# Kernel optimization log

Measured on AMD Instinct MI355X. Metric: run time of the kernel, lower is better.

## Reference

```python
import jax, jax.numpy as jnp
import numpy as np

THR = 0.5      # span-selection threshold
K_SUBJ = 16    # max subject/object spans kept per sentence (padded)
K_OBJ = 8      # max object spans kept per (subject, relation)

# Greedy threshold-based span pairing: for each start position i with
# start_prob>THR, take the first unused j>=i with end_prob>THR (NMS-like).
# Returns fixed-size padded spans [K,2] (int32) and a validity mask [K].
def greedy_spans(sp, ep, K):
    S = sp.shape[0]
    idxs = jnp.arange(S, dtype=jnp.int32)
    def step(carry, i):
        used, count, spans, valid = carry
        gate = sp[i] > THR
        cand = (ep > THR) & (~used) & (idxs >= i)
        has = jnp.any(cand)
        j = jnp.argmax(cand).astype(jnp.int32)  # first True
        found = gate & has
        slot = jnp.minimum(count, K - 1)
        write = found & (count < K)
        pair = jnp.where(write, jnp.stack([i, j]).astype(jnp.int32), spans[slot])
        spans = spans.at[slot].set(pair)
        valid = valid.at[slot].set(valid[slot] | write)
        used = used.at[j].set(used[j] | found)
        count = count + found.astype(jnp.int32)
        return (used, count, spans, valid), None
    init = (jnp.zeros(S, bool), jnp.int32(0),
            jnp.zeros((K, 2), jnp.int32), jnp.zeros(K, bool))
    (_, _, spans, valid), _ = jax.lax.scan(step, init, idxs)
    return spans, valid


def _model(token_embs, hg, rel_embs, b_rel_transe, head_w, head_b,
           Wmats, Wbias, rproj_w, rproj_b, V_w, V_b):
    # head_w/head_b order: 0 start_subj, 1 end_subj, 2 b_start_obj, 3 b_end_obj,
    #                      4 start_obj, 5 end_obj, 6 b_start_subj, 7 b_end_subj
    # Wmats/Wbias order:   0 W_s, 1 W_r, 2 W_g, 3 W_x, 4 W_r_b, 5 W_g_b, 6 W_x_b, 7 W_x2
    sig = jax.nn.sigmoid
    head = lambda x, i: sig(x @ head_w[i] + head_b[i])        # H->1 sigmoid head
    lin = lambda x, i: x @ Wmats[i].T + Wbias[i]              # H->H linear

    # ---- first-level span scores + greedy extraction (forward & backward) ----
    sub_sp, sub_ep = head(token_embs, 0), head(token_embs, 1)   # [B,S]
    bob_sp, bob_ep = head(token_embs, 2), head(token_embs, 3)
    g = jax.vmap(lambda a, b: greedy_spans(a, b, K_SUBJ))
    subj_spans, subj_valid = g(sub_sp, sub_ep)                  # [B,K,2],[B,K]
    b_subj_spans, b_subj_valid = g(bob_sp, bob_ep)

    def gather(tok_b, spans, valid):  # mean of start/end token embeddings
        e = (tok_b[spans[:, 0]] + tok_b[spans[:, 1]]) * 0.5
        return e * valid[:, None].astype(tok_b.dtype)
    s_k = jax.vmap(gather)(token_embs, subj_spans, subj_valid)      # [B,K,H]
    b_s_k = jax.vmap(gather)(token_embs, b_subj_spans, b_subj_valid)
    s_k_w = lin(s_k, 0) * subj_valid[..., None]                     # W_s + mask
    b_s_k_w = lin(b_s_k, 0) * b_subj_valid[..., None]

    # ---- relation-aware attention context C = sum_s A[b,s,r] * x[b,s] ----
    b_rel = b_rel_transe @ rproj_w.T + rproj_b                      # r_proj
    def attend(rels, ir, ig, ix):
        e = jnp.tanh(lin(token_embs, ix)[:, :, None, :]             # [B,S,1,H]
                     + lin(hg, ig)[:, None, None, :]                # [B,1,1,H]
                     + lin(rels, ir)[None, None, :, :])             # [1,1,R,H]
        v = e @ V_w + V_b[0]                                        # [B,S,R]
        A = jax.nn.softmax(v, axis=1)                               # over seq
        return jnp.einsum('bsr,bsh->brh', A, token_embs)            # [B,R,H]
    C = attend(rel_embs, 1, 2, 3)
    b_C = attend(b_rel, 4, 5, 6)

    # Heads are linear, so distribute w over the sum instead of
    # materializing the [B,S,K,R,H] tensor.
    tok_mix = token_embs + lin(token_embs, 7)
    def pair_probs(Cmat, skw, i):
        t_tok = tok_mix @ head_w[i]                                 # [B,S]
        t_sub = skw @ head_w[i]                                     # [B,K]
        t_rel = Cmat @ head_w[i]                                    # [B,R]
        return sig(t_tok[:, :, None, None] + t_sub[:, None, :, None]
                   + t_rel[:, None, None, :] + head_b[i])           # [B,S,K,R]
    obj_sp, obj_ep = pair_probs(C, s_k_w, 4), pair_probs(C, s_k_w, 5)
    bsub_sp, bsub_ep = pair_probs(b_C, b_s_k_w, 6), pair_probs(b_C, b_s_k_w, 7)

    # ---- greedy object-span extraction per (batch, subject, relation) ----
    def triples(sp4, ep4, subj_ok):
        B_, S_, K_, R_ = sp4.shape
        fsp = sp4.transpose(0, 2, 3, 1).reshape(-1, S_)
        fep = ep4.transpose(0, 2, 3, 1).reshape(-1, S_)
        spans, valid = jax.vmap(lambda a, b: greedy_spans(a, b, K_OBJ))(fsp, fep)
        spans = spans.reshape(B_, K_, R_, K_OBJ, 2)
        valid = valid.reshape(B_, K_, R_, K_OBJ) & subj_ok[:, :, None, None]
        return spans, valid
    f_spans, f_valid = triples(obj_sp, obj_ep, subj_valid)
    bw_spans, bw_valid = triples(bsub_sp, bsub_ep, b_subj_valid)

    probs = jnp.stack([obj_sp, obj_ep, bsub_sp, bsub_ep])           # [4,B,S,K,R]
    return (probs, subj_spans, subj_valid, b_subj_spans, b_subj_valid,
            f_spans, f_valid, bw_spans, bw_valid)


def setup_inputs() -> dict:
    key = jax.random.key(0)
    ks = jax.random.split(key, 12)
    B, S, H, R, T = 8, 256, 768, 40, 80
    sc = H ** -0.5
    return {
        'token_embs': jax.random.normal(ks[0], (B, S, H), jnp.float32),
        'hg': jax.random.normal(ks[1], (B, H), jnp.float32),
        'rel_embs': jax.random.normal(ks[2], (R, H), jnp.float32),
        'b_rel_transe': jax.random.normal(ks[3], (R, T), jnp.float32),
        'head_w': jax.random.normal(ks[4], (8, H), jnp.float32) * sc,
        'head_b': jax.random.normal(ks[5], (8,), jnp.float32) * 0.1,
        'Wmats': jax.random.normal(ks[6], (8, H, H), jnp.float32) * sc,
        'Wbias': jax.random.normal(ks[7], (8, H), jnp.float32) * 0.02,
        'rproj_w': jax.random.normal(ks[8], (H, T), jnp.float32) * (T ** -0.5),
        'rproj_b': jax.random.normal(ks[9], (H,), jnp.float32) * 0.02,
        'V_w': jax.random.normal(ks[10], (H,), jnp.float32) * sc,
        'V_b': jax.random.normal(ks[11], (1,), jnp.float32) * 0.1,
    }


def reference(token_embs, hg, rel_embs, b_rel_transe, head_w, head_b,
              Wmats, Wbias, rproj_w, rproj_b, V_w, V_b):
    return _model(token_embs, hg, rel_embs, b_rel_transe, head_w, head_b,
                  Wmats, Wbias, rproj_w, rproj_b, V_w, V_b)
```

## Files before the change

### kernel.cpp

```cpp
#include <hip/hip_runtime.h>
#include <hip/hip_bf16.h>
#include <stdint.h>

#define Bc 8
#define Sc 256
#define Hc 768
#define Rc 40
#define Tc 80
#define KSc 16
#define KOc 8

#define OUT_SSP 5242880
#define OUT_SVA 5243136
#define OUT_BSP 5243264
#define OUT_BVA 5243520
#define OUT_FSP 5243648
#define OUT_FVA 5325568
#define OUT_WSP 5366528
#define OUT_WVA 5448448

#define CM_PS (16 * Rc * Hc)
#define BSH (Bc * Sc * Hc)

__device__ inline double wave_reduce_d(double v) {
#pragma unroll
  for (int o = 32; o; o >>= 1) v += __shfl_down(v, o, 64);
  return v;
}
__device__ inline float wave_reduce_f(float v) {
#pragma unroll
  for (int o = 32; o; o >>= 1) v += __shfl_down(v, o, 64);
  return v;
}

__global__ __launch_bounds__(256) void k_prep0(const float* __restrict__ brt,
                                               const float* __restrict__ rw,
                                               const float* __restrict__ rb,
                                               const float* __restrict__ Wmats,
                                               const float* __restrict__ head_w,
                                               float* __restrict__ brel,
                                               double* __restrict__ hv) {
  int bb = blockIdx.x;
  int tid = threadIdx.x;
  if (bb < 12) {
    int idx = bb * 256 + tid;
    int i = idx / Hc, j = idx % Hc;
    const float* h4 = head_w + (4 + i) * Hc;
    const float* W7 = Wmats + (size_t)7 * Hc * Hc;
    double acc = (double)h4[j];
    for (int hh = 0; hh < Hc; ++hh)
      acc += (double)W7[(size_t)hh * Hc + j] * (double)h4[hh];
    hv[idx] = acc;
  } else {
    int idx = (bb - 12) * 256 + tid;
    int r = idx / Hc, h = idx % Hc;
    float acc = rb[h];
    const float* a = brt + r * Tc;
    const float* w = rw + (size_t)h * Tc;
    for (int t = 0; t < Tc; ++t) acc = fmaf(a[t], w[t], acc);
    brel[idx] = acc;
  }
}

__global__ __launch_bounds__(256) void k_l03tt(const float* __restrict__ x,
                                               const float* __restrict__ head_w,
                                               const float* __restrict__ head_b,
                                               const double* __restrict__ hv,
                                               float* __restrict__ l03,
                                               double* __restrict__ tt) {
  int bs = blockIdx.x * 4 + (threadIdx.x >> 6);
  int lane = threadIdx.x & 63;
  if (bs >= Bc * Sc) return;
  const float* xr = x + (size_t)bs * Hc;
  double acc[8] = {0, 0, 0, 0, 0, 0, 0, 0};
  for (int h = lane; h < Hc; h += 64) {
    double xv = (double)xr[h];
    acc[0] += xv * (double)head_w[h];
    acc[1] += xv * (double)head_w[Hc + h];
    acc[2] += xv * (double)head_w[2 * Hc + h];
    acc[3] += xv * (double)head_w[3 * Hc + h];
    acc[4] += xv * hv[h];
    acc[5] += xv * hv[Hc + h];
    acc[6] += xv * hv[2 * Hc + h];
    acc[7] += xv * hv[3 * Hc + h];
  }
#pragma unroll
  for (int i = 0; i < 4; ++i) {
    double a = wave_reduce_d(acc[i]);
    if (lane == 0) l03[i * (Bc * Sc) + bs] = (float)(a + (double)head_b[i]);
  }
#pragma unroll
  for (int i = 0; i < 4; ++i) {
    double a = wave_reduce_d(acc[4 + i]);
    if (lane == 0) tt[i * (Bc * Sc) + bs] = a;
  }
}

__device__ inline int find_first(const uint64_t* epm, const uint64_t* used, int i) {
  int wi = i >> 6;
  uint64_t m = epm[wi] & ~used[wi] & (~0ull << (i & 63));
  if (m) return (wi << 6) + (__ffsll((unsigned long long)m) - 1);
  for (int w = wi + 1; w < 4; ++w) {
    uint64_t mm = epm[w] & ~used[w];
    if (mm) return (w << 6) + (__ffsll((unsigned long long)mm) - 1);
  }
  return -1;
}

__global__ __launch_bounds__(64) void k_greedy1(const float* __restrict__ l03,
                                                int* __restrict__ spans1, int* __restrict__ valid1,
                                                float* __restrict__ out) {
  int t = blockIdx.x;
  int dir = t >> 3, b = t & 7;
  int lane = threadIdx.x;
  const float* sp = l03 + (dir * 2) * (Bc * Sc) + b * Sc;
  const float* ep = sp + Bc * Sc;
  uint64_t spm[4], epm[4];
#pragma unroll
  for (int w = 0; w < 4; ++w) {
    spm[w] = __ballot(sp[w * 64 + lane] > 0.f);
    epm[w] = __ballot(ep[w * 64 + lane] > 0.f);
  }
  __shared__ int ssp0[KSc], ssp1[KSc], sva[KSc];
  if (lane < KSc) { ssp0[lane] = 0; ssp1[lane] = 0; sva[lane] = 0; }
  __syncthreads();
  if (lane == 0) {
    uint64_t used[4] = {0, 0, 0, 0};
    int cnt = 0;
#pragma unroll
    for (int w = 0; w < 4; ++w) {
      uint64_t g = spm[w];
      while (g) {
        int bit = __ffsll((unsigned long long)g) - 1;
        g &= g - 1;
        int i = w * 64 + bit;
        int j = find_first(epm, used, i);
        if (j < 0) continue;
        used[j >> 6] |= (1ull << (j & 63));
        if (cnt < KSc) { ssp0[cnt] = i; ssp1[cnt] = j; sva[cnt] = 1; }
        cnt++;
      }
    }
  }
  __syncthreads();
  int base = (dir * Bc + b) * KSc;
  float* osp = out + (dir ? OUT_BSP : OUT_SSP) + b * KSc * 2;
  float* ova = out + (dir ? OUT_BVA : OUT_SVA) + b * KSc;
  if (lane < KSc) {
    spans1[(base + lane) * 2] = ssp0[lane];
    spans1[(base + lane) * 2 + 1] = ssp1[lane];
    valid1[base + lane] = sva[lane];
    osp[lane * 2] = (float)ssp0[lane];
    osp[lane * 2 + 1] = (float)ssp1[lane];
    ova[lane] = (float)sva[lane];
  }
}

__global__ __launch_bounds__(256) void k_egather(const float* __restrict__ x,
                                                 const int* __restrict__ spans1,
                                                 float* __restrict__ eb) {
  int row = blockIdx.x;
  int b = (row / KSc) % Bc;
  int s0 = spans1[row * 2], s1 = spans1[row * 2 + 1];
  const float* x0 = x + ((size_t)b * Sc + s0) * Hc;
  const float* x1 = x + ((size_t)b * Sc + s1) * Hc;
  float* er = eb + (size_t)row * Hc;
  for (int h = threadIdx.x; h < Hc; h += 256) er[h] = 0.5f * (x0[h] + x1[h]);
}

__global__ __launch_bounds__(256) void k_small(const float* __restrict__ eb,
                                               const float* __restrict__ hg,
                                               const float* __restrict__ rel,
                                               const float* __restrict__ brel,
                                               const float* __restrict__ Wmats,
                                               const float* __restrict__ Wbias,
                                               const int* __restrict__ valid1,
                                               float* __restrict__ skw,
                                               float* __restrict__ tg,
                                               float* __restrict__ tr) {
  int bb = blockIdx.x;
  const float* Asrc; int M; int wsel; float* dst; int m0, n0; bool msk = false;
  if (bb < 96) {
    Asrc = eb; M = 256; wsel = 0; dst = skw; msk = true;
    m0 = (bb / 12) * 32; n0 = (bb % 12) * 64;
  } else {
    int q = bb - 96;
    if (q < 12)      { Asrc = hg;   M = 8;  wsel = 2; dst = tg;           m0 = 0; n0 = q * 64; }
    else if (q < 24) { Asrc = hg;   M = 8;  wsel = 5; dst = tg + 8 * Hc;  m0 = 0; n0 = (q - 12) * 64; }
    else if (q < 48) { int qq = q - 24; Asrc = rel;  M = 40; wsel = 1; dst = tr;           m0 = (qq / 12) * 32; n0 = (qq % 12) * 64; }
    else             { int qq = q - 48; Asrc = brel; M = 40; wsel = 4; dst = tr + 40 * Hc; m0 = (qq / 12) * 32; n0 = (qq % 12) * 64; }
  }
  const float* W = Wmats + (size_t)wsel * Hc * Hc;
  const float* bias = Wbias + wsel * Hc;
  __shared__ float Asl[32][36];
  __shared__ float Bsl[32][68];
  int tid = threadIdx.x;
  int arow = tid >> 3, acol = (tid & 7) << 2;
  int brow = tid >> 2, bcol = (tid & 3) << 2;
  int txi = tid & 15, tyi = tid >> 4;
  int ar = m0 + arow;
  const float* ap = Asrc + (size_t)(ar < M ? ar : 0) * Hc + acol;
  const float* bp = W + (size_t)(n0 + brow) * Hc + bcol;
  int nb = n0 + txi * 4;
  float4 bv = *(const float4*)&bias[nb];
  float acc[2][4];
#pragma unroll
  for (int i = 0; i < 2; ++i) { acc[i][0] = bv.x; acc[i][1] = bv.y; acc[i][2] = bv.z; acc[i][3] = bv.w; }
  for (int k0 = 0; k0 < Hc; k0 += 32) {
    float4 av = *(const float4*)(ap + k0);
    float4 b0 = *(const float4*)(bp + k0);
    float4 b1 = *(const float4*)(bp + k0 + 16);
    __syncthreads();
    Asl[acol + 0][arow] = av.x; Asl[acol + 1][arow] = av.y; Asl[acol + 2][arow] = av.z; Asl[acol + 3][arow] = av.w;
    Bsl[bcol + 0][brow] = b0.x; Bsl[bcol + 1][brow] = b0.y; Bsl[bcol + 2][brow] = b0.z; Bsl[bcol + 3][brow] = b0.w;
    Bsl[bcol + 16][brow] = b1.x; Bsl[bcol + 17][brow] = b1.y; Bsl[bcol + 18][brow] = b1.z; Bsl[bcol + 19][brow] = b1.w;
    __syncthreads();
#pragma unroll
    for (int kk = 0; kk < 32; ++kk) {
      float a0 = Asl[kk][tyi * 2], a1 = Asl[kk][tyi * 2 + 1];
      float4 b = *(const float4*)&Bsl[kk][txi * 4];
      acc[0][0] = fmaf(a0, b.x, acc[0][0]); acc[0][1] = fmaf(a0, b.y, acc[0][1]);
      acc[0][2] = fmaf(a0, b.z, acc[0][2]); acc[0][3] = fmaf(a0, b.w, acc[0][3]);
      acc[1][0] = fmaf(a1, b.x, acc[1][0]); acc[1][1] = fmaf(a1, b.y, acc[1][1]);
      acc[1][2] = fmaf(a1, b.z, acc[1][2]); acc[1][3] = fmaf(a1, b.w, acc[1][3]);
    }
  }
  int m_ = m0 + tyi * 2;
#pragma unroll
  for (int i = 0; i < 2; ++i) {
    int mrow = m_ + i;
    if (msk) {
      int v = valid1[mrow];
      float4 o;
      o.x = v ? acc[i][0] : 0.f; o.y = v ? acc[i][1] : 0.f;
      o.z = v ? acc[i][2] : 0.f; o.w = v ? acc[i][3] : 0.f;
      *(float4*)&dst[(size_t)mrow * Hc + nb] = o;
    } else if (mrow < M) {
      float4 o; o.x = acc[i][0]; o.y = acc[i][1]; o.z = acc[i][2]; o.w = acc[i][3];
      *(float4*)&dst[(size_t)mrow * Hc + nb] = o;
    }
  }
}

#define BM 64
#define BN 64
#define BKK 32
#define LDP 68
__global__ __launch_bounds__(256) void k_tx(const float* __restrict__ x,
                                            const float* __restrict__ Wmats,
                                            const float* __restrict__ Wbias,
                                            float* __restrict__ txo) {
  int dir = blockIdx.z;
  const float* W = Wmats + (size_t)(dir ? 6 : 3) * Hc * Hc;
  const float* bias = Wbias + (dir ? 6 : 3) * Hc;
  float* outp = txo + (size_t)dir * BSH;
  int m0 = blockIdx.y * BM;
  int n0 = blockIdx.x * BN;
  __shared__ float Asl[BKK][LDP];
  __shared__ float Bsl[BKK][LDP];
  int tid = threadIdx.x;
  int lr = tid >> 2;
  int lc = (tid & 3) << 2;
  int txi = tid & 15, tyi = tid >> 4;
  const float* xp = x + (size_t)(m0 + lr) * Hc + lc;
  const float* wp = W + (size_t)(n0 + lr) * Hc + lc;
  float4 a0 = *(const float4*)(xp);
  float4 a1 = *(const float4*)(xp + 16);
  float4 b0 = *(const float4*)(wp);
  float4 b1 = *(const float4*)(wp + 16);
  float acc[4][4] = {};
  for (int k0 = 0; k0 < Hc; k0 += BKK) {
    __syncthreads();
    Asl[lc + 0][lr] = a0.x; Asl[lc + 1][lr] = a0.y; Asl[lc + 2][lr] = a0.z; Asl[lc + 3][lr] = a0.w;
    Asl[lc + 16][lr] = a1.x; Asl[lc + 17][lr] = a1.y; Asl[lc + 18][lr] = a1.z; Asl[lc + 19][lr] = a1.w;
    Bsl[lc + 0][lr] = b0.x; Bsl[lc + 1][lr] = b0.y; Bsl[lc + 2][lr] = b0.z; Bsl[lc + 3][lr] = b0.w;
    Bsl[lc + 16][lr] = b1.x; Bsl[lc + 17][lr] = b1.y; Bsl[lc + 18][lr] = b1.z; Bsl[lc + 19][lr] = b1.w;
    __syncthreads();
    if (k0 + BKK < Hc) {
      a0 = *(const float4*)(xp + k0 + BKK);
      a1 = *(const float4*)(xp + k0 + BKK + 16);
      b0 = *(const float4*)(wp + k0 + BKK);
      b1 = *(const float4*)(wp + k0 + BKK + 16);
    }
#pragma unroll
    for (int kk = 0; kk < BKK; ++kk) {
      float4 a = *(const float4*)&Asl[kk][tyi * 4];
      float4 b = *(const float4*)&Bsl[kk][txi * 4];
      acc[0][0] = fmaf(a.x, b.x, acc[0][0]); acc[0][1] = fmaf(a.x, b.y, acc[0][1]);
      acc[0][2] = fmaf(a.x, b.z, acc[0][2]); acc[0][3] = fmaf(a.x, b.w, acc[0][3]);
      acc[1][0] = fmaf(a.y, b.x, acc[1][0]); acc[1][1] = fmaf(a.y, b.y, acc[1][1]);
      acc[1][2] = fmaf(a.y, b.z, acc[1][2]); acc[1][3] = fmaf(a.y, b.w, acc[1][3]);
      acc[2][0] = fmaf(a.z, b.x, acc[2][0]); acc[2][1] = fmaf(a.z, b.y, acc[2][1]);
      acc[2][2] = fmaf(a.z, b.z, acc[2][2]); acc[2][3] = fmaf(a.z, b.w, acc[2][3]);
      acc[3][0] = fmaf(a.w, b.x, acc[3][0]); acc[3][1] = fmaf(a.w, b.y, acc[3][1]);
      acc[3][2] = fmaf(a.w, b.z, acc[3][2]); acc[3][3] = fmaf(a.w, b.w, acc[3][3]);
    }
  }
  int nb = n0 + txi * 4;
  float4 bb = *(const float4*)&bias[nb];
#pragma unroll
  for (int i2 = 0; i2 < 4; ++i2) {
    float4 o;
    o.x = acc[i2][0] + bb.x; o.y = acc[i2][1] + bb.y;
    o.z = acc[i2][2] + bb.z; o.w = acc[i2][3] + bb.w;
    *(float4*)&outp[(size_t)(m0 + tyi * 4 + i2) * Hc + nb] = o;
  }
}

__global__ __launch_bounds__(256) void k_v(const float* __restrict__ txo,
                                           const float* __restrict__ tg,
                                           const float* __restrict__ tr,
                                           const float* __restrict__ Vw,
                                           const float* __restrict__ Vb,
                                           float* __restrict__ va) {
  const float Cl = 2.8853900817779268f;
  int id = blockIdx.x;
  int dir = id >> 10;
  int rem = id & 1023;
  int rhalf = rem & 1;
  int bs0 = (rem >> 1) * 4;
  int b = bs0 >> 8;
  int tid = threadIdx.x;
  int wv = tid >> 6, lane = tid & 63;
  const float* tgr = tg + (dir * Bc + b) * Hc;
  float xt[4][12], vw[12];
#pragma unroll
  for (int u = 0; u < 12; ++u) {
    int h = lane + 64 * u;
    vw[u] = Vw[h];
    float tgv = tgr[h];
#pragma unroll
    for (int si = 0; si < 4; ++si)
      xt[si][u] = (txo[((size_t)dir * (Bc * Sc) + bs0 + si) * Hc + h] + tgv) * Cl;
  }
  float vb0 = Vb[0];
  for (int q = 0; q < 5; ++q) {
    int r = rhalf * 20 + wv * 5 + q;
    const float* trr = tr + ((size_t)dir * Rc + r) * Hc + lane;
    float p0 = 0.f, p1 = 0.f, p2 = 0.f, p3 = 0.f;
#pragma unroll
    for (int u = 0; u < 12; ++u) {
      float t = trr[64 * u] * Cl;
      float e0 = __builtin_amdgcn_exp2f(xt[0][u] + t);
      float e1 = __builtin_amdgcn_exp2f(xt[1][u] + t);
      float e2 = __builtin_amdgcn_exp2f(xt[2][u] + t);
      float e3 = __builtin_amdgcn_exp2f(xt[3][u] + t);
      p0 = fmaf(fmaf(-2.f, __builtin_amdgcn_rcpf(e0 + 1.f), 1.f), vw[u], p0);
      p1 = fmaf(fmaf(-2.f, __builtin_amdgcn_rcpf(e1 + 1.f), 1.f), vw[u], p1);
      p2 = fmaf(fmaf(-2.f, __builtin_amdgcn_rcpf(e2 + 1.f), 1.f), vw[u], p2);
      p3 = fmaf(fmaf(-2.f, __builtin_amdgcn_rcpf(e3 + 1.f), 1.f), vw[u], p3);
    }
    p0 = wave_reduce_f(p0); p1 = wave_reduce_f(p1);
    p2 = wave_reduce_f(p2); p3 = wave_reduce_f(p3);
    if (lane == 0) {
      size_t base = ((size_t)dir * (Bc * Sc) + bs0) * Rc + r;
      va[base] = p0 + vb0;
      va[base + Rc] = p1 + vb0;
      va[base + 2 * Rc] = p2 + vb0;
      va[base + 3 * Rc] = p3 + vb0;
    }
  }
}

__global__ __launch_bounds__(256) void k_softmax(float* __restrict__ va) {
  int id = blockIdx.x;
  int dir = id / (Bc * Rc); int rem = id % (Bc * Rc);
  int b = rem / Rc; int r = rem % Rc;
  int s = threadIdx.x;
  float* base = va + (((size_t)dir * Bc + b) * Sc) * Rc + r;
  float v = base[(size_t)s * Rc];
  __shared__ float red[8];
  float m = v;
#pragma unroll
  for (int o = 32; o; o >>= 1) m = fmaxf(m, __shfl_xor(m, o, 64));
  if ((s & 63) == 0) red[s >> 6] = m;
  __syncthreads();
  if (s == 0) red[4] = fmaxf(fmaxf(red[0], red[1]), fmaxf(red[2], red[3]));
  __syncthreads();
  m = red[4];
  float e = expf(v - m);
  float t = e;
#pragma unroll
  for (int o = 32; o; o >>= 1) t += __shfl_xor(t, o, 64);
  __syncthreads();
  if ((s & 63) == 0) red[s >> 6] = t;
  __syncthreads();
  if (s == 0) red[4] = red[0] + red[1] + red[2] + red[3];
  __syncthreads();
  base[(size_t)s * Rc] = e / red[4];
}

__global__ __launch_bounds__(256, 1) void k_C(const float* __restrict__ va,
                                              const float* __restrict__ x,
                                              float* __restrict__ Cm4) {
  int id = blockIdx.x;
  int rr = id & 1;
  int p = (id >> 1) & 3;
  int g = id >> 3;
  int b = g & 7;
  __shared__ float As_[64 * Rc];
  int tid = threadIdx.x;
  const float* vab = va + ((size_t)g * Sc + p * 64) * Rc;
  for (int idx = tid; idx < 64 * Rc; idx += 256) As_[idx] = vab[idx];
  __syncthreads();
  const float* xb = x + ((size_t)b * Sc + p * 64) * Hc;
  float acc[3][20];
#pragma unroll
  for (int j = 0; j < 3; ++j)
#pragma unroll
    for (int r = 0; r < 20; ++r) acc[j][r] = 0.f;
  int rbase = rr * 20;
  for (int s = 0; s < 64; ++s) {
    float xv0 = xb[(size_t)s * Hc + tid];
    float xv1 = xb[(size_t)s * Hc + 256 + tid];
    float xv2 = xb[(size_t)s * Hc + 512 + tid];
#pragma unroll
    for (int q = 0; q < 5; ++q) {
      float4 a4 = *(const float4*)&As_[s * Rc + rbase + q * 4];
      acc[0][q * 4 + 0] = fmaf(a4.x, xv0, acc[0][q * 4 + 0]);
      acc[0][q * 4 + 1] = fmaf(a4.y, xv0, acc[0][q * 4 + 1]);
      acc[0][q * 4 + 2] = fmaf(a4.z, xv0, acc[0][q * 4 + 2]);
      acc[0][q * 4 + 3] = fmaf(a4.w, xv0, acc[0][q * 4 + 3]);
      acc[1][q * 4 + 0] = fmaf(a4.x, xv1, acc[1][q * 4 + 0]);
      acc[1][q * 4 + 1] = fmaf(a4.y, xv1, acc[1][q * 4 + 1]);
      acc[1][q * 4 + 2] = fmaf(a4.z, xv1, acc[1][q * 4 + 2]);
      acc[1][q * 4 + 3] = fmaf(a4.w, xv1, acc[1][q * 4 + 3]);
      acc[2][q * 4 + 0] = fmaf(a4.x, xv2, acc[2][q * 4 + 0]);
      acc[2][q * 4 + 1] = fmaf(a4.y, xv2, acc[2][q * 4 + 1]);
      acc[2][q * 4 + 2] = fmaf(a4.z, xv2, acc[2][q * 4 + 2]);
      acc[2][q * 4 + 3] = fmaf(a4.w, xv2, acc[2][q * 4 + 3]);
    }
  }
#pragma unroll
  for (int r = 0; r < 20; ++r) {
    size_t base = ((size_t)(p * 16 + g) * Rc + rbase + r) * Hc + tid;
    Cm4[base] = acc[0][r];
    Cm4[base + 256] = acc[1][r];
    Cm4[base + 512] = acc[2][r];
  }
}

__global__ __launch_bounds__(256) void k_tsc(const float* __restrict__ skw,
                                             const float* __restrict__ Cm4,
                                             const float* __restrict__ head_w,
                                             const float* __restrict__ Wbias,
                                             double* __restrict__ ts,
                                             double* __restrict__ trl,
                                             double* __restrict__ c4) {
  int wave = blockIdx.x * 4 + (threadIdx.x >> 6);
  int lane = threadIdx.x & 63;
  const float* src; const float* w; double* dst;
  bool partial4 = false;
  if (wave < 512) {
    int p = wave >> 7, rem = wave & 127;
    int b = rem >> 4, k = rem & 15, dir = p >> 1;
    src = skw + (((size_t)(dir * Bc + b)) * KSc + k) * Hc;
    w = head_w + (4 + p) * Hc;
    dst = ts + (p * Bc + b) * KSc + k;
  } else if (wave < 1792) {
    int q = wave - 512;
    int p = q / 320, rem = q % 320;
    int b = rem / Rc, r = rem % Rc, dir = p >> 1;
    src = Cm4 + ((size_t)(dir * Bc + b) * Rc + r) * Hc;
    w = head_w + (4 + p) * Hc;
    dst = trl + (p * Bc + b) * Rc + r;
    partial4 = true;
  } else if (wave < 1796) {
    int p = wave - 1792;
    src = Wbias + 7 * Hc;
    w = head_w + (4 + p) * Hc;
    dst = c4 + p;
  } else return;
  double acc = 0.0;
  if (partial4) {
    for (int h = lane; h < Hc; h += 64) {
      double cs = (double)src[h] + (double)src[h + CM_PS] +
                  (double)src[h + 2 * CM_PS] + (double)src[h + 3 * CM_PS];
      acc += cs * (double)w[h];
    }
  } else {
    for (int h = lane; h < Hc; h += 64) acc += (double)src[h] * (double)w[h];
  }
  acc = wave_reduce_d(acc);
  if (lane == 0) *dst = acc;
}

__global__ __launch_bounds__(256) void k_probs(const double* __restrict__ tt,
                                               const double* __restrict__ ts,
                                               const double* __restrict__ trl,
                                               const double* __restrict__ c4,
                                               const float* __restrict__ head_b,
                                               float* __restrict__ out) {
  const float L2E = 1.4426950408889634f;
  int id = blockIdx.x;
  int b = id >> 8, s = id & 255;
  (void)s;
  __shared__ double tsb[4][KSc];
  __shared__ double trb[4][Rc];
  __shared__ double basep[4];
  int tid = threadIdx.x;
  if (tid < 64) { int p = tid >> 4, k = tid & 15; tsb[p][k] = ts[(p * Bc + b) * KSc + k]; }
  if (tid < 160) { int p = tid / Rc, r = tid % Rc; trb[p][r] = trl[(p * Bc + b) * Rc + r]; }
  if (tid < 4) basep[tid] = tt[tid * (Bc * Sc) + id] + c4[tid] + (double)head_b[4 + tid];
  __syncthreads();
#pragma unroll
  for (int p = 0; p < 4; ++p) {
    double base = basep[p];
    float* op = out + ((size_t)(p * Bc) * Sc + id) * (KSc * Rc);
    for (int kr = tid; kr < KSc * Rc; kr += 256) {
      int k = kr / Rc, r = kr - k * Rc;
      float l = (float)(base + tsb[p][k] + trb[p][r]);
      float e = __builtin_amdgcn_exp2f(-L2E * l);
      op[kr] = __builtin_amdgcn_rcpf(1.f + e);
    }
  }
}

__global__ __launch_bounds__(64) void k_greedy2(const double* __restrict__ tt,
                                                const double* __restrict__ ts,
                                                const double* __restrict__ trl,
                                                const double* __restrict__ c4,
                                                const float* __restrict__ head_b,
                                                const int* __restrict__ valid1,
                                                float* __restrict__ out) {
  int gid = blockIdx.x * 64 + threadIdx.x;
  if (gid >= 2 * Bc * KSc * Rc) return;
  int dir = gid / (Bc * KSc * Rc);
  int rem = gid % (Bc * KSc * Rc);
  int b = rem / (KSc * Rc);
  int kr = rem % (KSc * Rc);
  int k = kr / Rc, r = kr % Rc;
  int p0 = dir * 2, p1 = p0 + 1;
  double off0 = ts[(p0 * Bc + b) * KSc + k] + trl[(p0 * Bc + b) * Rc + r] + c4[p0] + (double)head_b[4 + p0];
  double off1 = ts[(p1 * Bc + b) * KSc + k] + trl[(p1 * Bc + b) * Rc + r] + c4[p1] + (double)head_b[4 + p1];
  const double* t0 = tt + p0 * (Bc * Sc) + b * Sc;
  const double* t1 = tt + p1 * (Bc * Sc) + b * Sc;
  uint64_t spm[4], epm[4], used[4] = {0, 0, 0, 0};
#pragma unroll
  for (int w = 0; w < 4; ++w) {
    uint64_t ms = 0, me = 0;
    for (int bit = 0; bit < 64; ++bit) {
      int s = w * 64 + bit;
      if (t0[s] + off0 > 0.0) ms |= (1ull << bit);
      if (t1[s] + off1 > 0.0) me |= (1ull << bit);
    }
    spm[w] = ms; epm[w] = me;
  }
  float* osp = out + (dir ? OUT_WSP : OUT_FSP) + (size_t)rem * KOc * 2;
  float* ova = out + (dir ? OUT_WVA : OUT_FVA) + (size_t)rem * KOc;
  for (int o = 0; o < KOc; ++o) { osp[o * 2] = 0.f; osp[o * 2 + 1] = 0.f; ova[o] = 0.f; }
  float sval = valid1[(dir * Bc + b) * KSc + k] ? 1.f : 0.f;
  int cnt = 0;
  for (int w = 0; w < 4; ++w) {
    uint64_t g = spm[w];
    while (g) {
      int bit = __ffsll((unsigned long long)g) - 1;
      g &= g - 1;
      int i = w * 64 + bit;
      int j = find_first(epm, used, i);
      if (j < 0) continue;
      used[j >> 6] |= (1ull << (j & 63));
      if (cnt < KOc) { osp[cnt * 2] = (float)i; osp[cnt * 2 + 1] = (float)j; ova[cnt] = sval; }
      cnt++;
    }
  }
}

extern "C" void kernel_launch(void* const* d_in, const int* in_sizes, int n_in,
                              void* d_out, int out_size, void* d_ws, size_t ws_size,
                              hipStream_t stream) {
  (void)in_sizes; (void)n_in; (void)out_size; (void)ws_size;
  const float* x = (const float*)d_in[0];
  const float* hg = (const float*)d_in[1];
  const float* rel = (const float*)d_in[2];
  const float* brt = (const float*)d_in[3];
  const float* head_w = (const float*)d_in[4];
  const float* head_b = (const float*)d_in[5];
  const float* Wmats = (const float*)d_in[6];
  const float* Wbias = (const float*)d_in[7];
  const float* rproj_w = (const float*)d_in[8];
  const float* rproj_b = (const float*)d_in[9];
  const float* Vw = (const float*)d_in[10];
  const float* Vb = (const float*)d_in[11];
  float* out = (float*)d_out;
  char* ws = (char*)d_ws;

  double* hv  = (double*)(ws + 0);
  double* c4  = (double*)(ws + 24576);
  double* tt  = (double*)(ws + 24608);
  double* ts  = (double*)(ws + 90144);
  double* trl = (double*)(ws + 94240);
  float* l03  = (float*)(ws + 104480);
  float* brel = (float*)(ws + 137248);
  float* tg   = (float*)(ws + 260128);
  float* tr   = (float*)(ws + 309280);
  float* txb  = (float*)(ws + 555040);
  float* va   = (float*)(ws + 13137952);
  float* skw  = (float*)(ws + 15759392);
  int* spans1 = (int*)(ws + 16545824);
  int* valid1 = (int*)(ws + 16547872);
  float* eb   = txb;
  float* Cm4  = txb;

  k_prep0<<<132, 256, 0, stream>>>(brt, rproj_w, rproj_b, Wmats, head_w, brel, hv);
  k_l03tt<<<512, 256, 0, stream>>>(x, head_w, head_b, hv, l03, tt);
  k_greedy1<<<16, 64, 0, stream>>>(l03, spans1, valid1, out);
  k_egather<<<256, 256, 0, stream>>>(x, spans1, eb);
  k_small<<<168, 256, 0, stream>>>(eb, hg, rel, brel, Wmats, Wbias, valid1, skw, tg, tr);
  k_tx<<<dim3(12, 32, 2), 256, 0, stream>>>(x, Wmats, Wbias, txb);
  k_v<<<2048, 256, 0, stream>>>(txb, tg, tr, Vw, Vb, va);
  k_softmax<<<640, 256, 0, stream>>>(va);
  k_C<<<128, 256, 0, stream>>>(va, x, Cm4);
  k_tsc<<<449, 256, 0, stream>>>(skw, Cm4, head_w, Wbias, ts, trl, c4);
  k_probs<<<2048, 256, 0, stream>>>(tt, ts, trl, c4, head_b, out);
  k_greedy2<<<160, 64, 0, stream>>>(tt, ts, trl, c4, head_b, valid1, out);
}
```

Baseline: 310.3 us.

## Fuse span gather into GEMM load and merge probs with greedy2 kernel

Drops the separate span-embedding gather kernel by computing the average of the two endpoint token rows directly inside the k_small GEMM's A-tile load. The sigmoid-probability kernel and the second greedy extraction kernel are merged into one launch, with extra blocks handling the greedy work at 256 threads per block instead of 64. This removes two kernel launches and the intermediate buffer write and read. In exchange, the GEMM issues two global loads per A element, and the greedy threads are now packed into fewer, larger blocks.

```diff
diff --git a/kernel.cpp b/kernel.cpp
--- a/kernel.cpp
+++ b/kernel.cpp
@@ -156,19 +156,8 @@
   }
 }
 
-__global__ __launch_bounds__(256) void k_egather(const float* __restrict__ x,
-                                                 const int* __restrict__ spans1,
-                                                 float* __restrict__ eb) {
-  int row = blockIdx.x;
-  int b = (row / KSc) % Bc;
-  int s0 = spans1[row * 2], s1 = spans1[row * 2 + 1];
-  const float* x0 = x + ((size_t)b * Sc + s0) * Hc;
-  const float* x1 = x + ((size_t)b * Sc + s1) * Hc;
-  float* er = eb + (size_t)row * Hc;
-  for (int h = threadIdx.x; h < Hc; h += 256) er[h] = 0.5f * (x0[h] + x1[h]);
-}
-
-__global__ __launch_bounds__(256) void k_small(const float* __restrict__ eb,
+__global__ __launch_bounds__(256) void k_small(const float* __restrict__ x,
+                                               const int* __restrict__ spans1,
                                                const float* __restrict__ hg,
                                                const float* __restrict__ rel,
                                                const float* __restrict__ brel,
@@ -179,9 +168,9 @@
                                                float* __restrict__ tg,
                                                float* __restrict__ tr) {
   int bb = blockIdx.x;
-  const float* Asrc; int M; int wsel; float* dst; int m0, n0; bool msk = false;
+  const float* Asrc = nullptr; int M; int wsel; float* dst; int m0, n0; bool msk = false;
   if (bb < 96) {
-    Asrc = eb; M = 256; wsel = 0; dst = skw; msk = true;
+    M = 256; wsel = 0; dst = skw; msk = true;
     m0 = (bb / 12) * 32; n0 = (bb % 12) * 64;
   } else {
     int q = bb - 96;
@@ -199,7 +188,17 @@
   int brow = tid >> 2, bcol = (tid & 3) << 2;
   int txi = tid & 15, tyi = tid >> 4;
   int ar = m0 + arow;
-  const float* ap = Asrc + (size_t)(ar < M ? ar : 0) * Hc + acol;
+  const float* ap = nullptr;
+  const float* apA = nullptr;
+  const float* apB = nullptr;
+  if (msk) {
+    int s0 = spans1[ar * 2], s1 = spans1[ar * 2 + 1];
+    int b = (ar >> 4) & 7;
+    apA = x + ((size_t)b * Sc + s0) * Hc + acol;
+    apB = x + ((size_t)b * Sc + s1) * Hc + acol;
+  } else {
+    ap = Asrc + (size_t)(ar < M ? ar : 0) * Hc + acol;
+  }
   const float* bp = W + (size_t)(n0 + brow) * Hc + bcol;
   int nb = n0 + txi * 4;
   float4 bv = *(const float4*)&bias[nb];
@@ -207,7 +206,15 @@
 #pragma unroll
   for (int i = 0; i < 2; ++i) { acc[i][0] = bv.x; acc[i][1] = bv.y; acc[i][2] = bv.z; acc[i][3] = bv.w; }
   for (int k0 = 0; k0 < Hc; k0 += 32) {
-    float4 av = *(const float4*)(ap + k0);
+    float4 av;
+    if (msk) {
+      float4 u = *(const float4*)(apA + k0);
+      float4 v = *(const float4*)(apB + k0);
+      av.x = 0.5f * (u.x + v.x); av.y = 0.5f * (u.y + v.y);
+      av.z = 0.5f * (u.z + v.z); av.w = 0.5f * (u.w + v.w);
+    } else {
+      av = *(const float4*)(ap + k0);
+    }
     float4 b0 = *(const float4*)(bp + k0);
     float4 b1 = *(const float4*)(bp + k0 + 16);
     __syncthreads();
@@ -485,83 +492,78 @@
   if (lane == 0) *dst = acc;
 }
 
-__global__ __launch_bounds__(256) void k_probs(const double* __restrict__ tt,
-                                               const double* __restrict__ ts,
-                                               const double* __restrict__ trl,
-                                               const double* __restrict__ c4,
-                                               const float* __restrict__ head_b,
-                                               float* __restrict__ out) {
+__global__ __launch_bounds__(256) void k_post(const double* __restrict__ tt,
+                                              const double* __restrict__ ts,
+                                              const double* __restrict__ trl,
+                                              const double* __restrict__ c4,
+                                              const float* __restrict__ head_b,
+                                              const int* __restrict__ valid1,
+                                              float* __restrict__ out) {
   const float L2E = 1.4426950408889634f;
-  int id = blockIdx.x;
-  int b = id >> 8, s = id & 255;
-  (void)s;
-  __shared__ double tsb[4][KSc];
-  __shared__ double trb[4][Rc];
-  __shared__ double basep[4];
+  int bb = blockIdx.x;
   int tid = threadIdx.x;
-  if (tid < 64) { int p = tid >> 4, k = tid & 15; tsb[p][k] = ts[(p * Bc + b) * KSc + k]; }
-  if (tid < 160) { int p = tid / Rc, r = tid % Rc; trb[p][r] = trl[(p * Bc + b) * Rc + r]; }
-  if (tid < 4) basep[tid] = tt[tid * (Bc * Sc) + id] + c4[tid] + (double)head_b[4 + tid];
-  __syncthreads();
-#pragma unroll
-  for (int p = 0; p < 4; ++p) {
-    double base = basep[p];
-    float* op = out + ((size_t)(p * Bc) * Sc + id) * (KSc * Rc);
-    for (int kr = tid; kr < KSc * Rc; kr += 256) {
-      int k = kr / Rc, r = kr - k * Rc;
-      float l = (float)(base + tsb[p][k] + trb[p][r]);
-      float e = __builtin_amdgcn_exp2f(-L2E * l);
-      op[kr] = __builtin_amdgcn_rcpf(1.f + e);
-    }
-  }
-}
-
-__global__ __launch_bounds__(64) void k_greedy2(const double* __restrict__ tt,
-                                                const double* __restrict__ ts,
-                                                const double* __restrict__ trl,
-                                                const double* __restrict__ c4,
-                                                const float* __restrict__ head_b,
-                                                const int* __restrict__ valid1,
-                                                float* __restrict__ out) {
-  int gid = blockIdx.x * 64 + threadIdx.x;
-  if (gid >= 2 * Bc * KSc * Rc) return;
-  int dir = gid / (Bc * KSc * Rc);
-  int rem = gid % (Bc * KSc * Rc);
-  int b = rem / (KSc * Rc);
-  int kr = rem % (KSc * Rc);
-  int k = kr / Rc, r = kr % Rc;
-  int p0 = dir * 2, p1 = p0 + 1;
-  double off0 = ts[(p0 * Bc + b) * KSc + k] + trl[(p0 * Bc + b) * Rc + r] + c4[p0] + (double)head_b[4 + p0];
-  double off1 = ts[(p1 * Bc + b) * KSc + k] + trl[(p1 * Bc + b) * Rc + r] + c4[p1] + (double)head_b[4 + p1];
-  const double* t0 = tt + p0 * (Bc * Sc) + b * Sc;
-  const double* t1 = tt + p1 * (Bc * Sc) + b * Sc;
-  uint64_t spm[4], epm[4], used[4] = {0, 0, 0, 0};
-#pragma unroll
-  for (int w = 0; w < 4; ++w) {
-    uint64_t ms = 0, me = 0;
-    for (int bit = 0; bit < 64; ++bit) {
-      int s = w * 64 + bit;
-      if (t0[s] + off0 > 0.0) ms |= (1ull << bit);
-      if (t1[s] + off1 > 0.0) me |= (1ull << bit);
-    }
-    spm[w] = ms; epm[w] = me;
-  }
-  float* osp = out + (dir ? OUT_WSP : OUT_FSP) + (size_t)rem * KOc * 2;
-  float* ova = out + (dir ? OUT_WVA : OUT_FVA) + (size_t)rem * KOc;
-  for (int o = 0; o < KOc; ++o) { osp[o * 2] = 0.f; osp[o * 2 + 1] = 0.f; ova[o] = 0.f; }
-  float sval = valid1[(dir * Bc + b) * KSc + k] ? 1.f : 0.f;
-  int cnt = 0;
-  for (int w = 0; w < 4; ++w) {
-    uint64_t g = spm[w];
-    while (g) {
-      int bit = __ffsll((unsigned long long)g) - 1;
-      g &= g - 1;
-      int i = w * 64 + bit;
-      int j = find_first(epm, used, i);
-      if (j < 0) continue;
-      used[j >> 6] |= (1ull << (j & 63));
-      if (cnt < KOc) { osp[cnt * 2] = (float)i; osp[cnt * 2 + 1] = (float)j; ova[cnt] = sval; }
-      cnt++;
+  if (bb < 2048) {
+    int id = bb;
+    int b = id >> 8;
+    __shared__ double tsb[4][KSc];
+    __shared__ double trb[4][Rc];
+    __shared__ double basep[4];
+    if (tid < 64) { int p = tid >> 4, k = tid & 15; tsb[p][k] = ts[(p * Bc + b) * KSc + k]; }
+    if (tid < 160) { int p = tid / Rc, r = tid % Rc; trb[p][r] = trl[(p * Bc + b) * Rc + r]; }
+    if (tid < 4) basep[tid] = tt[tid * (Bc * Sc) + id] + c4[tid] + (double)head_b[4 + tid];
+    __syncthreads();
+#pragma unroll
+    for (int p = 0; p < 4; ++p) {
+      double base = basep[p];
+      float* op = out + ((size_t)(p * Bc) * Sc + id) * (KSc * Rc);
+      for (int kr = tid; kr < KSc * Rc; kr += 256) {
+        int k = kr / Rc, r = kr - k * Rc;
+        float l = (float)(base + tsb[p][k] + trb[p][r]);
+        float e = __builtin_amdgcn_exp2f(-L2E * l);
+        op[kr] = __builtin_amdgcn_rcpf(1.f + e);
+      }
+    }
+  } else {
+    int gid = (bb - 2048) * 256 + tid;
+    if (gid >= 2 * Bc * KSc * Rc) return;
+    int dir = gid / (Bc * KSc * Rc);
+    int rem = gid % (Bc * KSc * Rc);
+    int b = rem / (KSc * Rc);
+    int kr = rem % (KSc * Rc);
+    int k = kr / Rc, r = kr % Rc;
+    int p0 = dir * 2, p1 = p0 + 1;
+    double off0 = ts[(p0 * Bc + b) * KSc + k] + trl[(p0 * Bc + b) * Rc + r] + c4[p0] + (double)head_b[4 + p0];
+    double off1 = ts[(p1 * Bc + b) * KSc + k] + trl[(p1 * Bc + b) * Rc + r] + c4[p1] + (double)head_b[4 + p1];
+    const double* t0 = tt + p0 * (Bc * Sc) + b * Sc;
+    const double* t1 = tt + p1 * (Bc * Sc) + b * Sc;
+    uint64_t spm[4], epm[4], used[4] = {0, 0, 0, 0};
+#pragma unroll
+    for (int w = 0; w < 4; ++w) {
+      uint64_t ms = 0, me = 0;
+      for (int bit = 0; bit < 64; ++bit) {
+        int s = w * 64 + bit;
+        if (t0[s] + off0 > 0.0) ms |= (1ull << bit);
+        if (t1[s] + off1 > 0.0) me |= (1ull << bit);
+      }
+      spm[w] = ms; epm[w] = me;
+    }
+    float* osp = out + (dir ? OUT_WSP : OUT_FSP) + (size_t)rem * KOc * 2;
+    float* ova = out + (dir ? OUT_WVA : OUT_FVA) + (size_t)rem * KOc;
+    for (int o = 0; o < KOc; ++o) { osp[o * 2] = 0.f; osp[o * 2 + 1] = 0.f; ova[o] = 0.f; }
+    float sval = valid1[(dir * Bc + b) * KSc + k] ? 1.f : 0.f;
+    int cnt = 0;
+    for (int w = 0; w < 4; ++w) {
+      uint64_t g = spm[w];
+      while (g) {
+        int bit = __ffsll((unsigned long long)g) - 1;
+        g &= g - 1;
+        int i = w * 64 + bit;
+        int j = find_first(epm, used, i);
+        if (j < 0) continue;
+        used[j >> 6] |= (1ull << (j & 63));
+        if (cnt < KOc) { osp[cnt * 2] = (float)i; osp[cnt * 2 + 1] = (float)j; ova[cnt] = sval; }
+        cnt++;
+      }
     }
   }
 }
@@ -599,19 +601,16 @@
   float* skw  = (float*)(ws + 15759392);
   int* spans1 = (int*)(ws + 16545824);
   int* valid1 = (int*)(ws + 16547872);
-  float* eb   = txb;
   float* Cm4  = txb;
 
   k_prep0<<<132, 256, 0, stream>>>(brt, rproj_w, rproj_b, Wmats, head_w, brel, hv);
   k_l03tt<<<512, 256, 0, stream>>>(x, head_w, head_b, hv, l03, tt);
   k_greedy1<<<16, 64, 0, stream>>>(l03, spans1, valid1, out);
-  k_egather<<<256, 256, 0, stream>>>(x, spans1, eb);
-  k_small<<<168, 256, 0, stream>>>(eb, hg, rel, brel, Wmats, Wbias, valid1, skw, tg, tr);
+  k_small<<<168, 256, 0, stream>>>(x, spans1, hg, rel, brel, Wmats, Wbias, valid1, skw, tg, tr);
   k_tx<<<dim3(12, 32, 2), 256, 0, stream>>>(x, Wmats, Wbias, txb);
   k_v<<<2048, 256, 0, stream>>>(txb, tg, tr, Vw, Vb, va);
   k_softmax<<<640, 256, 0, stream>>>(va);
   k_C<<<128, 256, 0, stream>>>(va, x, Cm4);
   k_tsc<<<449, 256, 0, stream>>>(skw, Cm4, head_w, Wbias, ts, trl, c4);
-  k_probs<<<2048, 256, 0, stream>>>(tt, ts, trl, c4, head_b, out);
-  k_greedy2<<<160, 64, 0, stream>>>(tt, ts, trl, c4, head_b, valid1, out);
-}
+  k_post<<<2088, 256, 0, stream>>>(tt, ts, trl, c4, head_b, valid1, out);
+}
```

Result: no change. 315.4 us (+1.6%).

## Restructure softmax to stage whole batch tile in LDS with coalesced IO

Applied to the files above, without the earlier changes.

The softmax kernel now launches one block per (direction, batch) group instead of one per (direction, batch, relation). Each block loads the full 256x40 slab into padded shared memory with coalesced reads and writes, and each wave handles 10 relations using register-held values and wave shuffles. It also swaps expf for exp2 with a log2e prescale. The aim is to remove strided 160-byte global accesses and block-level syncs, at the cost of only 16 blocks running on a large GPU, which may leave most CUs idle.

```diff
diff --git a/kernel.cpp b/kernel.cpp
--- a/kernel.cpp
+++ b/kernel.cpp
@@ -363,31 +363,45 @@
 }
 
 __global__ __launch_bounds__(256) void k_softmax(float* __restrict__ va) {
-  int id = blockIdx.x;
-  int dir = id / (Bc * Rc); int rem = id % (Bc * Rc);
-  int b = rem / Rc; int r = rem % Rc;
-  int s = threadIdx.x;
-  float* base = va + (((size_t)dir * Bc + b) * Sc) * Rc + r;
-  float v = base[(size_t)s * Rc];
-  __shared__ float red[8];
-  float m = v;
-#pragma unroll
-  for (int o = 32; o; o >>= 1) m = fmaxf(m, __shfl_xor(m, o, 64));
-  if ((s & 63) == 0) red[s >> 6] = m;
+  const float L2E = 1.4426950408889634f;
+  int g = blockIdx.x;
+  float* vab = va + (size_t)g * Sc * Rc;
+  __shared__ float sm[Sc * 41];
+  int tid = threadIdx.x;
+  for (int idx = tid; idx < Sc * Rc; idx += 256) {
+    int s = idx / Rc, r = idx - s * Rc;
+    sm[s * 41 + r] = vab[idx];
+  }
   __syncthreads();
-  if (s == 0) red[4] = fmaxf(fmaxf(red[0], red[1]), fmaxf(red[2], red[3]));
+  int wv = tid >> 6, lane = tid & 63;
+#pragma unroll
+  for (int q = 0; q < 10; ++q) {
+    int r = wv * 10 + q;
+    float v0 = sm[lane * 41 + r];
+    float v1 = sm[(lane + 64) * 41 + r];
+    float v2 = sm[(lane + 128) * 41 + r];
+    float v3 = sm[(lane + 192) * 41 + r];
+    float m = fmaxf(fmaxf(v0, v1), fmaxf(v2, v3));
+#pragma unroll
+    for (int o = 32; o; o >>= 1) m = fmaxf(m, __shfl_xor(m, o, 64));
+    float e0 = __builtin_amdgcn_exp2f((v0 - m) * L2E);
+    float e1 = __builtin_amdgcn_exp2f((v1 - m) * L2E);
+    float e2 = __builtin_amdgcn_exp2f((v2 - m) * L2E);
+    float e3 = __builtin_amdgcn_exp2f((v3 - m) * L2E);
+    float t = e0 + e1 + e2 + e3;
+#pragma unroll
+    for (int o = 32; o; o >>= 1) t += __shfl_xor(t, o, 64);
+    float inv = 1.f / t;
+    sm[lane * 41 + r] = e0 * inv;
+    sm[(lane + 64) * 41 + r] = e1 * inv;
+    sm[(lane + 128) * 41 + r] = e2 * inv;
+    sm[(lane + 192) * 41 + r] = e3 * inv;
+  }
   __syncthreads();
-  m = red[4];
-  float e = expf(v - m);
-  float t = e;
-#pragma unroll
-  for (int o = 32; o; o >>= 1) t += __shfl_xor(t, o, 64);
-  __syncthreads();
-  if ((s & 63) == 0) red[s >> 6] = t;
-  __syncthreads();
-  if (s == 0) red[4] = red[0] + red[1] + red[2] + red[3];
-  __syncthreads();
-  base[(size_t)s * Rc] = e / red[4];
+  for (int idx = tid; idx < Sc * Rc; idx += 256) {
+    int s = idx / Rc, r = idx - s * Rc;
+    vab[idx] = sm[s * 41 + r];
+  }
 }
 
 __global__ __launch_bounds__(256, 1) void k_C(const float* __restrict__ va,
@@ -609,7 +623,7 @@
   k_small<<<168, 256, 0, stream>>>(eb, hg, rel, brel, Wmats, Wbias, valid1, skw, tg, tr);
   k_tx<<<dim3(12, 32, 2), 256, 0, stream>>>(x, Wmats, Wbias, txb);
   k_v<<<2048, 256, 0, stream>>>(txb, tg, tr, Vw, Vb, va);
-  k_softmax<<<640, 256, 0, stream>>>(va);
+  k_softmax<<<16, 256, 0, stream>>>(va);
   k_C<<<128, 256, 0, stream>>>(va, x, Cm4);
   k_tsc<<<449, 256, 0, stream>>>(skw, Cm4, head_w, Wbias, ts, trl, c4);
   k_probs<<<2048, 256, 0, stream>>>(tt, ts, trl, c4, head_b, out);
```

Result: no change. 313.7 us (+1.1%).
